# Kernel optimization log

Measured on AMD Instinct MI355X. Metric: run time of the kernel, lower is better.

Reference implementation:

```python
import jax, jax.numpy as jnp
import numpy as np

N = 50000      # nodes
E = 60000      # edges
F_IN = 32      # num_features
DIM = 64       # hidden dim
B = 256        # graphs in batch


def setup_inputs() -> dict:
    key = jax.random.key(0)
    ks = jax.random.split(key, 18)
    s = 0.05
    rn = lambda k, shp: (jax.random.normal(k, shp, jnp.float32) * s)
    return {
        "x": jax.random.normal(ks[0], (N, F_IN), jnp.float32),
        "edge_index": jax.random.randint(ks[1], (2, E), 0, N),
        "batch": jnp.sort(jax.random.randint(ks[2], (N,), 0, B)),
        "lin0_w": rn(ks[3], (DIM, F_IN)), "lin0_b": rn(ks[4], (DIM,)),
        "nn1_w": rn(ks[5], (DIM, 1)), "nn1_b": rn(ks[6], (DIM,)),
        "nn2_w": rn(ks[7], (DIM * DIM, DIM)), "nn2_b": rn(ks[8], (DIM * DIM,)),
        "conv_b": rn(ks[9], (DIM,)),
        "gru_w_ih": rn(ks[10], (3 * DIM, DIM)), "gru_w_hh": rn(ks[11], (3 * DIM, DIM)),
        "gru_b_ih": rn(ks[12], (3 * DIM,)), "gru_b_hh": rn(ks[13], (3 * DIM,)),
        "lstm_w_ih": rn(ks[14], (4 * DIM, 2 * DIM)), "lstm_w_hh": rn(ks[15], (4 * DIM, DIM)),
        "lstm_b_ih": rn(ks[16], (4 * DIM,)), "lstm_b_hh": rn(ks[17], (4 * DIM,)),
    }


def reference(x, edge_index, batch, lin0_w, lin0_b, nn1_w, nn1_b, nn2_w, nn2_b,
              conv_b, gru_w_ih, gru_w_hh, gru_b_ih, gru_b_hh,
              lstm_w_ih, lstm_w_hh, lstm_b_ih, lstm_b_hh):
    src, dst = edge_index[0], edge_index[1]
    n_nodes = x.shape[0]
    out = jax.nn.relu(x @ lin0_w.T + lin0_b)          # [N, DIM]
    h = out                                            # GRU hidden state
    edge_attr = jnp.ones((edge_index.shape[1], 1), x.dtype)  # as in source forward
    ones_e = jnp.ones((edge_index.shape[1],), x.dtype)
    deg = jax.ops.segment_sum(ones_e, dst, num_segments=n_nodes)
    inv_deg = jnp.where(deg > 0, 1.0 / jnp.maximum(deg, 1.0), 0.0)[:, None]

    for _ in range(3):
        # edge-conditioned weight: MLP(edge_attr) -> [E, DIM, DIM]
        ew = (jax.nn.relu(edge_attr @ nn1_w.T + nn1_b) @ nn2_w.T + nn2_b)
        ew = ew.reshape(-1, DIM, DIM)
        msg = jnp.einsum('ei,eio->eo', out[src], ew)   # per-edge matvec
        agg = jax.ops.segment_sum(msg, dst, num_segments=n_nodes) * inv_deg  # scatter-mean
        m = jax.nn.relu(agg + conv_b)
        # GRU cell (seq_len = 1)
        gi = m @ gru_w_ih.T + gru_b_ih
        gh = h @ gru_w_hh.T + gru_b_hh
        i_r, i_z, i_n = jnp.split(gi, 3, axis=-1)
        h_r, h_z, h_n = jnp.split(gh, 3, axis=-1)
        r = jax.nn.sigmoid(i_r + h_r)
        z = jax.nn.sigmoid(i_z + h_z)
        n = jnp.tanh(i_n + r * h_n)
        h = (1.0 - z) * n + z * h
        out = h
    feat_map = out

    # Set2Set pooling, 3 processing steps, LSTM(2*DIM -> DIM)
    q_star = jnp.zeros((B, 2 * DIM), x.dtype)
    hl = jnp.zeros((B, DIM), x.dtype)
    cl = jnp.zeros((B, DIM), x.dtype)
    for _ in range(3):
        gates = q_star @ lstm_w_ih.T + lstm_b_ih + hl @ lstm_w_hh.T + lstm_b_hh
        ig, fg, gg, og = jnp.split(gates, 4, axis=-1)  # torch gate order i,f,g,o
        cl = jax.nn.sigmoid(fg) * cl + jax.nn.sigmoid(ig) * jnp.tanh(gg)
        hl = jax.nn.sigmoid(og) * jnp.tanh(cl)
        e = jnp.sum(out * hl[batch], axis=-1)          # [N]
        emax = jax.ops.segment_max(e, batch, num_segments=B)
        emax = jnp.where(jnp.isfinite(emax), emax, 0.0)
        a = jnp.exp(e - emax[batch])
        asum = jax.ops.segment_sum(a, batch, num_segments=B)
        a = a / (asum[batch] + 1e-16)                  # segment softmax
        r_vec = jax.ops.segment_sum(a[:, None] * out, batch, num_segments=B)
        q_star = jnp.concatenate([hl, r_vec], axis=-1)
    return q_star, feat_map
```

## Files before the change

kernel.cpp:

```cpp
#include <hip/hip_runtime.h>
#include <math.h>

#define NN 50000
#define NE 60000
#define FIN 32
#define DIM 64
#define NGB 256
#define SCB 196

typedef short s8v __attribute__((ext_vector_type(8)));
typedef float f4v __attribute__((ext_vector_type(4)));

__device__ __forceinline__ float rl(float v, int lane) {
    return __int_as_float(__builtin_amdgcn_readlane(__float_as_int(v), lane));
}
__device__ __forceinline__ float sigm(float x) { return 1.f / (1.f + expf(-x)); }

__device__ __forceinline__ unsigned int pk2(float a, float b) {
    unsigned int ua = __float_as_uint(a);
    unsigned int ub = __float_as_uint(b);
    ua = (ua + 0x7FFFu + ((ua >> 16) & 1u)) >> 16;
    ub = (ub + 0x7FFFu + ((ub >> 16) & 1u)) & 0xFFFF0000u;
    return ua | ub;
}
__device__ __forceinline__ unsigned short pk1(float a) {
    unsigned int ua = __float_as_uint(a);
    return (unsigned short)((ua + 0x7FFFu + ((ua >> 16) & 1u)) >> 16);
}
__device__ __forceinline__ s8v as_s8(uint4 u) {
    union { uint4 a; s8v b; } c; c.a = u; return c.b;
}

__global__ void k_precompute_W(const float* __restrict__ nn1_w, const float* __restrict__ nn1_b,
                               const float* __restrict__ nn2_w, const float* __restrict__ nn2_b,
                               float* __restrict__ W) {
    __shared__ float t[64];
    int tid = threadIdx.x;
    if (tid < 64) t[tid] = fmaxf(nn1_w[tid] + nn1_b[tid], 0.f);
    __syncthreads();
    int k = blockIdx.x * blockDim.x + tid;
    float acc = nn2_b[k];
    #pragma unroll
    for (int j = 0; j < 64; ++j) acc += t[j] * nn2_w[k * 64 + j];
    W[k] = acc;
}

__global__ void k_pack_mfma(const float* __restrict__ W, const float* __restrict__ wih,
                            const float* __restrict__ whh, const float* __restrict__ bih,
                            const float* __restrict__ bhh, unsigned int* __restrict__ P,
                            float* __restrict__ brz) {
    int q = blockIdx.x * 256 + threadIdx.x;
    if (q < 128) brz[q] = bih[q] + bhh[q];
    if (q < 2048) {
        int byte = q * 4, col = byte >> 7, rem = byte & 127;
        int lin = rem ^ ((col & 7) << 4);
        int k0 = (lin >> 4) * 8 + ((lin >> 2) & 3) * 2;
        P[q] = pk2(W[k0 * 64 + col], W[(k0 + 1) * 64 + col]);
    } else if (q < 10240) {
        int w = q - 2048, byte = w * 4, col = byte >> 8, rem = byte & 255;
        int lin = rem ^ ((col & 7) << 4);
        int k0 = (lin >> 4) * 8 + ((lin >> 2) & 3) * 2;
        int g = col >> 6, o = col & 63;
        int rowbase = (g * 64 + o) * 64;
        const float* src = (k0 >= 64) ? whh : wih;
        int kk = (k0 >= 64) ? k0 - 64 : k0;
        P[q] = pk2(src[rowbase + kk], src[rowbase + kk + 1]);
    } else if (q < 12288) {
        int w = q - 10240, byte = w * 4, col = byte >> 7, rem = byte & 127;
        int lin = rem ^ ((col & 7) << 4);
        int k0 = (lin >> 4) * 8 + ((lin >> 2) & 3) * 2;
        P[q] = pk2(wih[(128 + col) * 64 + k0], wih[(128 + col) * 64 + k0 + 1]);
    } else {
        int w = q - 12288, byte = w * 4, col = byte >> 7, rem = byte & 127;
        int lin = rem ^ ((col & 7) << 4);
        int k0 = (lin >> 4) * 8 + ((lin >> 2) & 3) * 2;
        P[q] = pk2(whh[(128 + col) * 64 + k0], whh[(128 + col) * 64 + k0 + 1]);
    }
}

__global__ void k_transpose_lstm(const float* __restrict__ wih, const float* __restrict__ whh,
                                 float* __restrict__ wihT, float* __restrict__ whhT) {
    int p = blockIdx.x * 256 + threadIdx.x;
    if (p < 256 * 128) { int o = p >> 7, k = p & 127; wihT[k * 256 + o] = wih[p]; }
    if (p < 256 * 64)  { int o = p >> 6, k = p & 63;  whhT[k * 256 + o] = whh[p]; }
}

__global__ void k_degi(const int* __restrict__ ei, int* __restrict__ degc) {
    int i = blockIdx.x * 256 + threadIdx.x;
    if (i < NE) atomicAdd(&degc[ei[NE + i]], 1);
}

__global__ void k_bsum(const int* __restrict__ degc, int* __restrict__ bsum) {
    __shared__ int red[256];
    int t = threadIdx.x;
    int idx = blockIdx.x * 256 + t;
    red[t] = (idx < NN) ? degc[idx] : 0;
    __syncthreads();
    for (int off = 128; off; off >>= 1) {
        if (t < off) red[t] += red[t + off];
        __syncthreads();
    }
    if (t == 0) bsum[blockIdx.x] = red[0];
}

__global__ void k_emit(const int* __restrict__ degc, const int* __restrict__ bsum,
                       int* __restrict__ rowptr, int* __restrict__ cur) {
    __shared__ int bo[256];
    __shared__ int sc[256];
    int t = threadIdx.x;
    int idx = blockIdx.x * 256 + t;
    bo[t] = (t < blockIdx.x) ? bsum[t] : 0;
    __syncthreads();
    for (int off = 128; off; off >>= 1) {
        if (t < off) bo[t] += bo[t + off];
        __syncthreads();
    }
    int boff = bo[0];
    int v = (idx < NN) ? degc[idx] : 0;
    sc[t] = v;
    __syncthreads();
    for (int off = 1; off < 256; off <<= 1) {
        int u = (t >= off) ? sc[t - off] : 0;
        __syncthreads();
        sc[t] += u;
        __syncthreads();
    }
    if (idx <= NN) {
        int excl = boff + sc[t] - v;
        rowptr[idx] = excl;
        if (idx < NN) cur[idx] = excl;
    }
}

__global__ void k_fill(const int* __restrict__ ei, int* __restrict__ cur,
                       int* __restrict__ adj) {
    int i = blockIdx.x * 256 + threadIdx.x;
    if (i < NE) {
        int s = ei[i], d = ei[NE + i];
        int pos = atomicAdd(&cur[d], 1);
        adj[pos] = s;
    }
}

__global__ void k_bounds(const int* __restrict__ batch, int* __restrict__ starts,
                         int* __restrict__ cnt) {
    __shared__ int sLB[257];
    int b = threadIdx.x;
    int lo = 0, hi = NN;
    while (lo < hi) {
        int mid = (lo + hi) >> 1;
        if (batch[mid] < b) lo = mid + 1; else hi = mid;
    }
    sLB[b] = lo;
    if (b == 0) sLB[256] = NN;
    __syncthreads();
    starts[b] = sLB[b];
    cnt[b] = sLB[b + 1] - sLB[b];
}

__global__ void k_lin0(const float* __restrict__ x, const float* __restrict__ w,
                       const float* __restrict__ b, float* __restrict__ h) {
    __shared__ float wT[FIN * 64];
    int tid = threadIdx.x;
    for (int p = tid; p < FIN * 64; p += 256) {
        int k = p >> 6, o = p & 63;
        wT[p] = w[o * FIN + k];
    }
    __syncthreads();
    int l = tid & 63;
    float bl = b[l];
    int wave = blockIdx.x * 4 + (tid >> 6);
    int nwaves = gridDim.x * 4;
    for (int n0 = wave * 2; n0 < NN; n0 += nwaves * 2) {
        float xv0 = x[n0 * FIN + (l & 31)];
        float xv1 = x[(n0 + 1) * FIN + (l & 31)];
        float a0 = bl, a1 = bl;
        #pragma unroll
        for (int k = 0; k < FIN; ++k) {
            float wk = wT[k * 64 + l];
            a0 += rl(xv0, k) * wk;
            a1 += rl(xv1, k) * wk;
        }
        h[n0 * 64 + l] = fmaxf(a0, 0.f);
        h[(n0 + 1) * 64 + l] = fmaxf(a1, 0.f);
    }
}

__global__ void __launch_bounds__(256) k_gather(const int* __restrict__ rowptr,
                                                const int* __restrict__ adj,
                                                const float* __restrict__ h,
                                                float* __restrict__ agg) {
    int gid = blockIdx.x * 256 + threadIdx.x;
    if (gid >= NN * 16) return;
    int n = gid >> 4, c = gid & 15;
    int s = rowptr[n], e = rowptr[n + 1];
    float4 acc = {0.f, 0.f, 0.f, 0.f};
    for (int k = s; k < e; ++k) {
        int src = adj[k];
        float4 v = *(const float4*)(h + src * 64 + c * 4);
        acc.x += v.x; acc.y += v.y; acc.z += v.z; acc.w += v.w;
    }
    *(float4*)(agg + n * 64 + c * 4) = acc;
}

__global__ void __launch_bounds__(256) k_update(
    const float* __restrict__ agg, const int* __restrict__ rowptr,
    const unsigned int* __restrict__ P, const float* __restrict__ conv_b,
    const float* __restrict__ brz, const float* __restrict__ bih, const float* __restrict__ bhh,
    float* __restrict__ h) {
    __shared__ unsigned int L[16384];
    int tid = threadIdx.x;
    #pragma unroll
    for (int p = 0; p < 14336; p += 256) L[p + tid] = P[p + tid];
    __syncthreads();

    int l = tid & 63;
    int w = tid >> 6;
    int nb = (blockIdx.x * 4 + w) * 16;
    if (nb >= NN) return;
    int row = l & 15, kq = l >> 4;
    int node = nb + row;

    float dv = (float)(rowptr[node + 1] - rowptr[node]);
    float inv = dv > 0.f ? 1.f / dv : 0.f;

    uint4 aA[2];
    #pragma unroll
    for (int kt = 0; kt < 2; ++kt) {
        const float4* src = (const float4*)(agg + node * 64 + kt * 32 + kq * 8);
        float4 x0 = src[0], x1 = src[1];
        aA[kt].x = pk2(x0.x * inv, x0.y * inv);
        aA[kt].y = pk2(x0.z * inv, x0.w * inv);
        aA[kt].z = pk2(x1.x * inv, x1.y * inv);
        aA[kt].w = pk2(x1.z * inv, x1.w * inv);
    }

    f4v mC[4];
    #pragma unroll
    for (int ct = 0; ct < 4; ++ct) {
        f4v acc = {0.f, 0.f, 0.f, 0.f};
        int col = ct * 16 + row;
        #pragma unroll
        for (int kt = 0; kt < 2; ++kt) {
            int boff = col * 128 + ((kt * 64 + kq * 16) ^ ((col & 7) << 4));
            uint4 b = *(const uint4*)((const char*)L + boff);
            acc = __builtin_amdgcn_mfma_f32_16x16x32_bf16(as_s8(aA[kt]), as_s8(b), acc, 0, 0, 0);
        }
        mC[ct] = acc;
    }

    int mbase = 57344 + w * 2048;
    #pragma unroll
    for (int ct = 0; ct < 4; ++ct) {
        int ch = ct * 16 + row;
        float cb = conv_b[ch];
        #pragma unroll
        for (int r = 0; r < 4; ++r) {
            float mval = fmaxf(mC[ct][r] + cb, 0.f);
            int nrow = kq * 4 + r;
            int off = mbase + ((nrow * 128 + ch * 2) ^ ((nrow & 7) << 4));
            *(unsigned short*)((char*)L + off) = pk1(mval);
        }
    }
    uint4 mA[2], hA[2];
    #pragma unroll
    for (int kt = 0; kt < 2; ++kt) {
        int off = mbase + ((row * 128 + kt * 64 + kq * 16) ^ ((row & 7) << 4));
        mA[kt] = *(const uint4*)((const char*)L + off);
        const float4* hs = (const float4*)(h + node * 64 + kt * 32 + kq * 8);
        float4 y0 = hs[0], y1 = hs[1];
        hA[kt].x = pk2(y0.x, y0.y);
        hA[kt].y = pk2(y0.z, y0.w);
        hA[kt].z = pk2(y1.x, y1.y);
        hA[kt].w = pk2(y1.z, y1.w);
    }

    f4v g01[8];
    #pragma unroll
    for (int ct = 0; ct < 8; ++ct) {
        f4v acc = {0.f, 0.f, 0.f, 0.f};
        int col = ct * 16 + row;
        #pragma unroll
        for (int kt = 0; kt < 4; ++kt) {
            uint4 a = (kt < 2) ? mA[kt] : hA[kt - 2];
            int boff = 8192 + col * 256 + ((kt * 64 + kq * 16) ^ ((col & 7) << 4));
            uint4 b = *(const uint4*)((const char*)L + boff);
            acc = __builtin_amdgcn_mfma_f32_16x16x32_bf16(as_s8(a), as_s8(b), acc, 0, 0, 0);
        }
        g01[ct] = acc;
    }
    f4v gin[4], ghn[4];
    #pragma unroll
    for (int ct = 0; ct < 4; ++ct) {
        f4v ai = {0.f, 0.f, 0.f, 0.f}, ah = {0.f, 0.f, 0.f, 0.f};
        int col = ct * 16 + row;
        #pragma unroll
        for (int kt = 0; kt < 2; ++kt) {
            int swz = (kt * 64 + kq * 16) ^ ((col & 7) << 4);
            uint4 bi = *(const uint4*)((const char*)L + 40960 + col * 128 + swz);
            uint4 bh = *(const uint4*)((const char*)L + 49152 + col * 128 + swz);
            ai = __builtin_amdgcn_mfma_f32_16x16x32_bf16(as_s8(mA[kt]), as_s8(bi), ai, 0, 0, 0);
            ah = __builtin_amdgcn_mfma_f32_16x16x32_bf16(as_s8(hA[kt]), as_s8(bh), ah, 0, 0, 0);
        }
        gin[ct] = ai; ghn[ct] = ah;
    }

    #pragma unroll
    for (int ct = 0; ct < 4; ++ct) {
        int ch = ct * 16 + row;
        float br = brz[ch], bz = brz[64 + ch];
        float bin = bih[128 + ch], bhn = bhh[128 + ch];
        #pragma unroll
        for (int r = 0; r < 4; ++r) {
            int n2 = nb + kq * 4 + r;
            float rg = sigm(g01[ct][r] + br);
            float zg = sigm(g01[4 + ct][r] + bz);
            float ng = tanhf(gin[ct][r] + bin + rg * (ghn[ct][r] + bhn));
            float hold = h[n2 * 64 + ch];
            h[n2 * 64 + ch] = (1.f - zg) * ng + zg * hold;
        }
    }
}

__global__ void __launch_bounds__(1024) k_s2s(
    const float* __restrict__ h, const int* __restrict__ starts,
    const int* __restrict__ cnt, const float* __restrict__ wihT,
    const float* __restrict__ whhT, const float* __restrict__ bih,
    const float* __restrict__ bhh, float* __restrict__ hl,
    float* __restrict__ cl, float* __restrict__ qstar, int first) {
    __shared__ float ga[256];
    __shared__ float hlv[64];
    __shared__ float mw[16], ssw[16];
    __shared__ float accw[16][64];
    int b = blockIdx.x, tid = threadIdx.x, w = tid >> 6, l = tid & 63;

    if (first) {
        if (tid < 64) {
            float ig = sigm(bih[tid] + bhh[tid]);
            float gg = tanhf(bih[128 + tid] + bhh[128 + tid]);
            float og = sigm(bih[192 + tid] + bhh[192 + tid]);
            float c = ig * gg;
            cl[b * 64 + tid] = c;
            float hh = og * tanhf(c);
            hl[b * 64 + tid] = hh;
            hlv[tid] = hh;
        }
    } else {
        if (tid < 256) {
            const float* qs = qstar + b * 128;
            const float* hb = hl + b * 64;
            float a = bih[tid] + bhh[tid];
            for (int k = 0; k < 128; ++k) a += qs[k] * wihT[k * 256 + tid];
            for (int k = 0; k < 64; ++k)  a += hb[k] * whhT[k * 256 + tid];
            ga[tid] = a;
        }
        __syncthreads();
        if (tid < 64) {
            float c = sigm(ga[64 + tid]) * cl[b * 64 + tid] + sigm(ga[tid]) * tanhf(ga[128 + tid]);
            cl[b * 64 + tid] = c;
            float hh = sigm(ga[192 + tid]) * tanhf(c);
            hl[b * 64 + tid] = hh;
            hlv[tid] = hh;
        }
    }
    __syncthreads();

    int s = starts[b], c = cnt[b];
    float hld = hlv[l];
    float m = -1e30f, ss = 0.f, racc = 0.f;
    for (int i = w; i < c; i += 16) {
        float hv = h[(s + i) * 64 + l];
        float v = hv * hld;
        #pragma unroll
        for (int off = 32; off; off >>= 1) v += __shfl_xor(v, off, 64);
        float nm = fmaxf(m, v);
        float scale = expf(m - nm);
        float p = expf(v - nm);
        ss = ss * scale + p;
        racc = racc * scale + p * hv;
        m = nm;
    }
    if (l == 0) { mw[w] = m; ssw[w] = ss; }
    accw[w][l] = racc;
    __syncthreads();
    if (tid < 64) {
        float M = -1e30f;
        #pragma unroll
        for (int q = 0; q < 16; ++q) M = fmaxf(M, mw[q]);
        float asum = 0.f, r = 0.f;
        #pragma unroll
        for (int q = 0; q < 16; ++q) {
            float f = expf(mw[q] - M);
            asum += ssw[q] * f;
            r += accw[q][tid] * f;
        }
        qstar[b * 128 + tid] = hlv[tid];
        qstar[b * 128 + 64 + tid] = r / (asum + 1e-16f);
    }
}

extern "C" void kernel_launch(void* const* d_in, const int* in_sizes, int n_in,
                              void* d_out, int out_size, void* d_ws, size_t ws_size,
                              hipStream_t stream) {
    const float* x      = (const float*)d_in[0];
    const int*   ei     = (const int*)  d_in[1];
    const int*   batch  = (const int*)  d_in[2];
    const float* lin0_w = (const float*)d_in[3];
    const float* lin0_b = (const float*)d_in[4];
    const float* nn1_w  = (const float*)d_in[5];
    const float* nn1_b  = (const float*)d_in[6];
    const float* nn2_w  = (const float*)d_in[7];
    const float* nn2_b  = (const float*)d_in[8];
    const float* conv_b = (const float*)d_in[9];
    const float* gwih   = (const float*)d_in[10];
    const float* gwhh   = (const float*)d_in[11];
    const float* gbih   = (const float*)d_in[12];
    const float* gbhh   = (const float*)d_in[13];
    const float* lwih   = (const float*)d_in[14];
    const float* lwhh   = (const float*)d_in[15];
    const float* lbih   = (const float*)d_in[16];
    const float* lbhh   = (const float*)d_in[17];

    float* qstar = (float*)d_out;
    float* h     = (float*)d_out + NGB * 128;

    float* ws     = (float*)d_ws;
    float* W      = ws;
    float* agg    = ws + 4096;
    int*   rowptr = (int*)(agg + NN * 64);
    int*   curp   = rowptr + NN + 1;
    int*   adj    = curp + NN;
    int*   degc   = adj + NE;
    int*   bsum   = degc + NN;
    int*   cnt    = bsum + 256;
    int*   starts = cnt + 256;
    float* hl     = (float*)(starts + 256);
    float* cl     = hl + NGB * 64;
    float* wihT   = cl + NGB * 64;
    float* whhT   = wihT + 128 * 256;
    unsigned int* P = (unsigned int*)(whhT + 64 * 256);
    float* brz    = (float*)(P + 14336);

    hipMemsetAsync(degc, 0, NN * sizeof(int), stream);

    k_precompute_W<<<16, 256, 0, stream>>>(nn1_w, nn1_b, nn2_w, nn2_b, W);
    k_pack_mfma<<<56, 256, 0, stream>>>(W, gwih, gwhh, gbih, gbhh, P, brz);
    k_transpose_lstm<<<128, 256, 0, stream>>>(lwih, lwhh, wihT, whhT);
    k_degi<<<(NE + 255) / 256, 256, 0, stream>>>(ei, degc);
    k_bsum<<<SCB, 256, 0, stream>>>(degc, bsum);
    k_emit<<<SCB, 256, 0, stream>>>(degc, bsum, rowptr, curp);
    k_fill<<<(NE + 255) / 256, 256, 0, stream>>>(ei, curp, adj);
    k_bounds<<<1, 256, 0, stream>>>(batch, starts, cnt);
    k_lin0<<<512, 256, 0, stream>>>(x, lin0_w, lin0_b, h);

    for (int it = 0; it < 3; ++it) {
        k_gather<<<(NN * 16 + 255) / 256, 256, 0, stream>>>(rowptr, adj, h, agg);
        k_update<<<782, 256, 0, stream>>>(agg, rowptr, P, conv_b, brz, gbih, gbhh, h);
    }
    for (int st = 0; st < 3; ++st) {
        k_s2s<<<NGB, 1024, 0, stream>>>(h, starts, cnt, wihT, whhT, lbih, lbhh,
                                        hl, cl, qstar, st == 0 ? 1 : 0);
    }
}
```

Measured before the change: 270.3 us.

## Fuse neighbor gather into GRU update kernel with ping-pong hidden buffers

Removes the separate gather kernel and folds the CSR neighbor sum into the update kernel, so each lane accumulates its own 16 feature slots directly in registers before packing them to bf16 MFMA operands. This drops three launches and the write and re-read of the 12.8 MB agg buffer each iteration. Because the update now reads neighbor states while writing new ones, the hidden state ping-pongs between a workspace buffer and the output buffer. The cost is that each lane now loads four float4s per edge, which are less coalesced than the old gather, and the per-wave imbalance in neighbor counts now stalls the MFMA work.

```diff
diff --git a/kernel.cpp b/kernel.cpp
--- a/kernel.cpp
+++ b/kernel.cpp
@@ -186,28 +186,12 @@
     }
 }
 
-__global__ void __launch_bounds__(256) k_gather(const int* __restrict__ rowptr,
-                                                const int* __restrict__ adj,
-                                                const float* __restrict__ h,
-                                                float* __restrict__ agg) {
-    int gid = blockIdx.x * 256 + threadIdx.x;
-    if (gid >= NN * 16) return;
-    int n = gid >> 4, c = gid & 15;
-    int s = rowptr[n], e = rowptr[n + 1];
-    float4 acc = {0.f, 0.f, 0.f, 0.f};
-    for (int k = s; k < e; ++k) {
-        int src = adj[k];
-        float4 v = *(const float4*)(h + src * 64 + c * 4);
-        acc.x += v.x; acc.y += v.y; acc.z += v.z; acc.w += v.w;
-    }
-    *(float4*)(agg + n * 64 + c * 4) = acc;
-}
-
 __global__ void __launch_bounds__(256) k_update(
-    const float* __restrict__ agg, const int* __restrict__ rowptr,
-    const unsigned int* __restrict__ P, const float* __restrict__ conv_b,
-    const float* __restrict__ brz, const float* __restrict__ bih, const float* __restrict__ bhh,
-    float* __restrict__ h) {
+    const float* __restrict__ hin, const int* __restrict__ rowptr,
+    const int* __restrict__ adj, const unsigned int* __restrict__ P,
+    const float* __restrict__ conv_b, const float* __restrict__ brz,
+    const float* __restrict__ bih, const float* __restrict__ bhh,
+    float* __restrict__ hout) {
     __shared__ unsigned int L[16384];
     int tid = threadIdx.x;
     #pragma unroll
@@ -221,19 +205,33 @@
     int row = l & 15, kq = l >> 4;
     int node = nb + row;
 
-    float dv = (float)(rowptr[node + 1] - rowptr[node]);
+    int es = rowptr[node], ee = rowptr[node + 1];
+    float g0x = 0.f, g0y = 0.f, g0z = 0.f, g0w = 0.f;
+    float g1x = 0.f, g1y = 0.f, g1z = 0.f, g1w = 0.f;
+    float g2x = 0.f, g2y = 0.f, g2z = 0.f, g2w = 0.f;
+    float g3x = 0.f, g3y = 0.f, g3z = 0.f, g3w = 0.f;
+    for (int k = es; k < ee; ++k) {
+        int src = adj[k];
+        const float4* hp0 = (const float4*)(hin + src * 64 + kq * 8);
+        const float4* hp1 = (const float4*)(hin + src * 64 + 32 + kq * 8);
+        float4 v0 = hp0[0], v1 = hp0[1], v2 = hp1[0], v3 = hp1[1];
+        g0x += v0.x; g0y += v0.y; g0z += v0.z; g0w += v0.w;
+        g1x += v1.x; g1y += v1.y; g1z += v1.z; g1w += v1.w;
+        g2x += v2.x; g2y += v2.y; g2z += v2.z; g2w += v2.w;
+        g3x += v3.x; g3y += v3.y; g3z += v3.z; g3w += v3.w;
+    }
+    float dv = (float)(ee - es);
     float inv = dv > 0.f ? 1.f / dv : 0.f;
 
     uint4 aA[2];
-    #pragma unroll
-    for (int kt = 0; kt < 2; ++kt) {
-        const float4* src = (const float4*)(agg + node * 64 + kt * 32 + kq * 8);
-        float4 x0 = src[0], x1 = src[1];
-        aA[kt].x = pk2(x0.x * inv, x0.y * inv);
-        aA[kt].y = pk2(x0.z * inv, x0.w * inv);
-        aA[kt].z = pk2(x1.x * inv, x1.y * inv);
-        aA[kt].w = pk2(x1.z * inv, x1.w * inv);
-    }
+    aA[0].x = pk2(g0x * inv, g0y * inv);
+    aA[0].y = pk2(g0z * inv, g0w * inv);
+    aA[0].z = pk2(g1x * inv, g1y * inv);
+    aA[0].w = pk2(g1z * inv, g1w * inv);
+    aA[1].x = pk2(g2x * inv, g2y * inv);
+    aA[1].y = pk2(g2z * inv, g2w * inv);
+    aA[1].z = pk2(g3x * inv, g3y * inv);
+    aA[1].w = pk2(g3z * inv, g3w * inv);
 
     f4v mC[4];
     #pragma unroll
@@ -267,7 +265,7 @@
     for (int kt = 0; kt < 2; ++kt) {
         int off = mbase + ((row * 128 + kt * 64 + kq * 16) ^ ((row & 7) << 4));
         mA[kt] = *(const uint4*)((const char*)L + off);
-        const float4* hs = (const float4*)(h + node * 64 + kt * 32 + kq * 8);
+        const float4* hs = (const float4*)(hin + node * 64 + kt * 32 + kq * 8);
         float4 y0 = hs[0], y1 = hs[1];
         hA[kt].x = pk2(y0.x, y0.y);
         hA[kt].y = pk2(y0.z, y0.w);
@@ -316,8 +314,8 @@
             float rg = sigm(g01[ct][r] + br);
             float zg = sigm(g01[4 + ct][r] + bz);
             float ng = tanhf(gin[ct][r] + bin + rg * (ghn[ct][r] + bhn));
-            float hold = h[n2 * 64 + ch];
-            h[n2 * 64 + ch] = (1.f - zg) * ng + zg * hold;
+            float hold = hin[n2 * 64 + ch];
+            hout[n2 * 64 + ch] = (1.f - zg) * ng + zg * hold;
         }
     }
 }
@@ -422,12 +420,12 @@
     const float* lbhh   = (const float*)d_in[17];
 
     float* qstar = (float*)d_out;
-    float* h     = (float*)d_out + NGB * 128;
+    float* hdo   = (float*)d_out + NGB * 128;
 
     float* ws     = (float*)d_ws;
     float* W      = ws;
-    float* agg    = ws + 4096;
-    int*   rowptr = (int*)(agg + NN * 64);
+    float* hbuf   = ws + 4096;
+    int*   rowptr = (int*)(hbuf + NN * 64);
     int*   curp   = rowptr + NN + 1;
     int*   adj    = curp + NN;
     int*   degc   = adj + NE;
@@ -451,14 +449,14 @@
     k_emit<<<SCB, 256, 0, stream>>>(degc, bsum, rowptr, curp);
     k_fill<<<(NE + 255) / 256, 256, 0, stream>>>(ei, curp, adj);
     k_bounds<<<1, 256, 0, stream>>>(batch, starts, cnt);
-    k_lin0<<<512, 256, 0, stream>>>(x, lin0_w, lin0_b, h);
-
-    for (int it = 0; it < 3; ++it) {
-        k_gather<<<(NN * 16 + 255) / 256, 256, 0, stream>>>(rowptr, adj, h, agg);
-        k_update<<<782, 256, 0, stream>>>(agg, rowptr, P, conv_b, brz, gbih, gbhh, h);
-    }
+    k_lin0<<<512, 256, 0, stream>>>(x, lin0_w, lin0_b, hbuf);
+
+    k_update<<<782, 256, 0, stream>>>(hbuf, rowptr, adj, P, conv_b, brz, gbih, gbhh, hdo);
+    k_update<<<782, 256, 0, stream>>>(hdo, rowptr, adj, P, conv_b, brz, gbih, gbhh, hbuf);
+    k_update<<<782, 256, 0, stream>>>(hbuf, rowptr, adj, P, conv_b, brz, gbih, gbhh, hdo);
+
     for (int st = 0; st < 3; ++st) {
-        k_s2s<<<NGB, 1024, 0, stream>>>(h, starts, cnt, wihT, whhT, lbih, lbhh,
+        k_s2s<<<NGB, 1024, 0, stream>>>(hdo, starts, cnt, wihT, whhT, lbih, lbhh,
                                         hl, cl, qstar, st == 0 ? 1 : 0);
     }
 }
```

Result: faster. 250.6 us (-7.3%).
